# Kernel optimization log

Hardware: AMD Instinct MI355X
Metric: run time of the kernel (lower is better)

Reference implementation:

```python
import jax, jax.numpy as jnp
import numpy as np

H = 8          # num heads
LN_EPS = 1e-5  # torch LayerNorm default

_SHAPES = {
    'src': (1024, 8, 256), 'pos': (1024, 8, 256), 'query_embed': (80, 8, 256), 'cam_mask': (8, 80, 1024),
    'enc_qkv_w': (2, 768, 256), 'enc_qkv_b': (2, 768), 'enc_out_w': (2, 256, 256), 'enc_out_b': (2, 256),
    'enc_ln1_g': (2, 256), 'enc_ln1_b': (2, 256),
    'enc_ff1_w': (2, 2048, 256), 'enc_ff1_b': (2, 2048), 'enc_ff2_w': (2, 256, 2048), 'enc_ff2_b': (2, 256),
    'enc_ln2_g': (2, 256), 'enc_ln2_b': (2, 256),
    'dec_sa_qkv_w': (2, 768, 256), 'dec_sa_qkv_b': (2, 768), 'dec_sa_out_w': (2, 256, 256), 'dec_sa_out_b': (2, 256),
    'dec_ln1_g': (2, 256), 'dec_ln1_b': (2, 256),
    'dec_ca_qkv_w': (2, 768, 256), 'dec_ca_qkv_b': (2, 768), 'dec_ca_out_w': (2, 256, 256), 'dec_ca_out_b': (2, 256),
    'dec_ln2_g': (2, 256), 'dec_ln2_b': (2, 256),
    'dec_ff1_w': (2, 2048, 256), 'dec_ff1_b': (2, 2048), 'dec_ff2_w': (2, 256, 2048), 'dec_ff2_b': (2, 256),
    'dec_ln3_g': (2, 256), 'dec_ln3_b': (2, 256),
    'dec_norm_g': (256,), 'dec_norm_b': (256,),
}


def setup_inputs() -> dict:
    key = jax.random.key(0)
    out = {}
    for i, (name, sh) in enumerate(_SHAPES.items()):
        k = jax.random.fold_in(key, i)
        if name.endswith('_g'):
            out[name] = jnp.ones(sh, jnp.float32)
        elif name.endswith('ln1_b') or name.endswith('ln2_b') or name.endswith('ln3_b') or name == 'dec_norm_b':
            out[name] = jnp.zeros(sh, jnp.float32)
        else:
            scale = 1.0 if name in ('src', 'pos', 'query_embed', 'cam_mask') else 0.02
            out[name] = jax.random.normal(k, sh, dtype=jnp.float32) * scale
    return out


def layer_norm(x, g, b):
    mu = jnp.mean(x, axis=-1, keepdims=True)
    var = jnp.mean(jnp.square(x - mu), axis=-1, keepdims=True)
    return (x - mu) * jax.lax.rsqrt(var + LN_EPS) * g + b


def mha(q_in, k_in, v_in, qkv_w, qkv_b, out_w, out_b, bias=None):
    # q_in: [L,B,D], k_in/v_in: [S,B,D]; torch layout: projections are x @ W.T + b
    L, B, D = q_in.shape
    S = k_in.shape[0]
    hd = D // H
    wq, wk, wv = qkv_w[:D], qkv_w[D:2 * D], qkv_w[2 * D:]
    bq, bk, bv = qkv_b[:D], qkv_b[D:2 * D], qkv_b[2 * D:]
    q = (q_in @ wq.T + bq).reshape(L, B, H, hd).transpose(1, 2, 0, 3)  # [B,H,L,hd]
    k = (k_in @ wk.T + bk).reshape(S, B, H, hd).transpose(1, 2, 0, 3)  # [B,H,S,hd]
    v = (v_in @ wv.T + bv).reshape(S, B, H, hd).transpose(1, 2, 0, 3)
    logits = jnp.einsum('bhld,bhsd->bhls', q, k) * (1.0 / np.sqrt(hd))
    if bias is not None:
        logits = logits + bias[:, None, :, :]  # CAM bias broadcast over heads
    attn = jax.nn.softmax(logits, axis=-1)
    o = jnp.einsum('bhls,bhsd->bhld', attn, v).transpose(2, 0, 1, 3).reshape(L, B, D)
    return o @ out_w.T + out_b


def reference(src, pos, query_embed, cam_mask,
              enc_qkv_w, enc_qkv_b, enc_out_w, enc_out_b, enc_ln1_g, enc_ln1_b,
              enc_ff1_w, enc_ff1_b, enc_ff2_w, enc_ff2_b, enc_ln2_g, enc_ln2_b,
              dec_sa_qkv_w, dec_sa_qkv_b, dec_sa_out_w, dec_sa_out_b, dec_ln1_g, dec_ln1_b,
              dec_ca_qkv_w, dec_ca_qkv_b, dec_ca_out_w, dec_ca_out_b, dec_ln2_g, dec_ln2_b,
              dec_ff1_w, dec_ff1_b, dec_ff2_w, dec_ff2_b, dec_ln3_g, dec_ln3_b,
              dec_norm_g, dec_norm_b):
    n_enc = enc_qkv_w.shape[0]
    n_dec = dec_sa_qkv_w.shape[0]
    # --- encoder (post-norm DETR style, pos added to q,k) ---
    mem = src
    for i in range(n_enc):
        qk = mem + pos
        a = mha(qk, qk, mem, enc_qkv_w[i], enc_qkv_b[i], enc_out_w[i], enc_out_b[i])
        mem = layer_norm(mem + a, enc_ln1_g[i], enc_ln1_b[i])
        f = jax.nn.relu(mem @ enc_ff1_w[i].T + enc_ff1_b[i]) @ enc_ff2_w[i].T + enc_ff2_b[i]
        mem = layer_norm(mem + f, enc_ln2_g[i], enc_ln2_b[i])
    # --- decoder: tgt starts at zeros (Q2L), query_embed is query_pos ---
    tgt = jnp.zeros_like(query_embed)
    for i in range(n_dec):
        qk = tgt + query_embed
        sa = mha(qk, qk, tgt, dec_sa_qkv_w[i], dec_sa_qkv_b[i], dec_sa_out_w[i], dec_sa_out_b[i])
        tgt = layer_norm(tgt + sa, dec_ln1_g[i], dec_ln1_b[i])
        ca = mha(tgt + query_embed, mem + pos, mem,
                 dec_ca_qkv_w[i], dec_ca_qkv_b[i], dec_ca_out_w[i], dec_ca_out_b[i],
                 bias=cam_mask)  # MA: CAM-derived additive attention bias [B,L,S]
        tgt = layer_norm(tgt + ca, dec_ln2_g[i], dec_ln2_b[i])
        f = jax.nn.relu(tgt @ dec_ff1_w[i].T + dec_ff1_b[i]) @ dec_ff2_w[i].T + dec_ff2_b[i]
        tgt = layer_norm(tgt + f, dec_ln3_g[i], dec_ln3_b[i])
    out = layer_norm(tgt, dec_norm_g, dec_norm_b)
    return out[None]  # [1, L, B, D] as in TransformerDecoder's output.unsqueeze(0)
```

## Files before the change

### kernel.cpp

```cpp
#include <hip/hip_runtime.h>
#include <hip/hip_bf16.h>
#include <cstdint>
#include <cstddef>

typedef __hip_bfloat16 bf16;
typedef float f4 __attribute__((ext_vector_type(4)));
typedef float f32x4 __attribute__((ext_vector_type(4)));
typedef short s8v __attribute__((ext_vector_type(8)));
typedef unsigned short u16x4 __attribute__((ext_vector_type(4)));
typedef unsigned short u16x8 __attribute__((ext_vector_type(8)));

#define LN_EPS 1e-5f
#define LOG2E 1.4426950408889634f

#if __has_builtin(__builtin_amdgcn_exp2f)
__device__ __forceinline__ float EXP2(float x) { return __builtin_amdgcn_exp2f(x); }
#else
__device__ __forceinline__ float EXP2(float x) {
  float r; asm("v_exp_f32 %0, %1" : "=v"(r) : "v"(x)); return r;
}
#endif

__device__ __forceinline__ void async_cp16(const void* g, void* lds) {
  __builtin_amdgcn_global_load_lds(
      (const __attribute__((address_space(1))) unsigned int*)g,
      (__attribute__((address_space(3))) unsigned int*)lds, 16, 0, 0);
}

__device__ __forceinline__ uint32_t pkbf(float lo, float hi) {
#if __has_builtin(__builtin_amdgcn_perm)
  uint32_t l = __builtin_bit_cast(uint32_t, lo) + 0x8000u;
  uint32_t h = __builtin_bit_cast(uint32_t, hi) + 0x8000u;
  return __builtin_amdgcn_perm(h, l, 0x07060302u);
#else
  uint32_t l = __builtin_bit_cast(uint32_t, lo) + 0x8000u;
  uint32_t h = __builtin_bit_cast(uint32_t, hi) + 0x8000u;
  return (l >> 16) | (h & 0xFFFF0000u);
#endif
}

#define NCAST 16
struct CastArgs {
  const float* in[NCAST];
  bf16* out[NCAST];
  int end4[NCAST];
  int nseg;
};

__global__ __launch_bounds__(256) void cast_multi(CastArgs a, int total4) {
  int i = blockIdx.x * 256 + threadIdx.x;
  if (i >= total4) return;
  int s = 0;
  while (i >= a.end4[s]) ++s;
  int j = i - (s ? a.end4[s - 1] : 0);
  f4 v = ((const f4*)a.in[s])[j];
  u16x4 o;
#pragma unroll
  for (int c = 0; c < 4; ++c) {
    bf16 h = __float2bfloat16(v[c]);
    o[c] = *reinterpret_cast<unsigned short*>(&h);
  }
  ((u16x4*)a.out[s])[j] = o;
}

__global__ __launch_bounds__(256) void scale_f32_kernel(const float* __restrict__ in,
                                                        float* __restrict__ out,
                                                        float s, int n4) {
  int i = blockIdx.x * 256 + threadIdx.x;
  if (i < n4) {
    f4 v = ((const f4*)in)[i];
    ((f4*)out)[i] = v * s;
  }
}

__global__ __launch_bounds__(256) void add_bf16_kernel(const float* __restrict__ a,
                                                       const float* __restrict__ b,
                                                       bf16* __restrict__ out, int n4) {
  int i = blockIdx.x * 256 + threadIdx.x;
  if (i < n4) {
    f4 x = ((const f4*)a)[i];
    f4 y = ((const f4*)b)[i];
    u16x4 o;
#pragma unroll
    for (int j = 0; j < 4; ++j) {
      bf16 h = __float2bfloat16(x[j] + y[j]);
      o[j] = *reinterpret_cast<unsigned short*>(&h);
    }
    ((u16x4*)out)[i] = o;
  }
}

template <int TB, int MODE, int SPLITK>
__global__ __launch_bounds__(256, 2) void mfma_gemm(
    const bf16* __restrict__ A, const bf16* __restrict__ W,
    const float* __restrict__ bias, float* __restrict__ C,
    bf16* __restrict__ Cb, int M, int N, int K, int HL, float qscale) {
  constexpr int WM = TB / 2, WN = TB / 2;
  constexpr int MR = WM / 16, NR = WN / 16;
  constexpr int NCH = TB / 32;
  __shared__ __attribute__((aligned(16))) unsigned short SH[TB * 128];
  unsigned short (*As)[64] = (unsigned short(*)[64])SH;
  unsigned short (*Ws)[64] = (unsigned short(*)[64])(SH + TB * 64);
  const int tid = threadIdx.x;
  const int lane = tid & 63, wave = tid >> 6;
  const int wr = wave >> 1, wc = wave & 1;
  const int bm = blockIdx.x * TB, bn = blockIdx.y * TB;
  const int fr = lane & 15, fo = lane >> 4;
  const int srowi = lane >> 3;
  const int slot = lane & 7;
  const int gcol = (slot ^ srowi) * 8;

  const int kchunk = K / SPLITK;
  const int kbeg = (SPLITK > 1) ? blockIdx.z * kchunk : 0;

  f32x4 acc[MR][NR] = {};

  for (int k0 = kbeg; k0 < kbeg + kchunk; k0 += 64) {
    __syncthreads();
#pragma unroll
    for (int c = 0; c < NCH; ++c) {
      int rbase = wave * (TB / 4) + c * 8;
      int row = rbase + srowi;
      async_cp16(A + (size_t)(bm + row) * K + k0 + gcol, &As[rbase][0]);
      async_cp16(W + (size_t)(bn + row) * K + k0 + gcol, &Ws[rbase][0]);
    }
    __syncthreads();
#pragma unroll
    for (int ks = 0; ks < 2; ++ks) {
      s8v a[MR], b[NR];
#pragma unroll
      for (int mi = 0; mi < MR; ++mi) {
        int row = wr * WM + mi * 16 + fr;
        a[mi] = *(const s8v*)((const char*)&As[0][0] + row * 128 +
                              ((ks * 64 + fo * 16) ^ ((row & 7) << 4)));
      }
#pragma unroll
      for (int ni = 0; ni < NR; ++ni) {
        int row = wc * WN + ni * 16 + fr;
        b[ni] = *(const s8v*)((const char*)&Ws[0][0] + row * 128 +
                              ((ks * 64 + fo * 16) ^ ((row & 7) << 4)));
      }
#pragma unroll
      for (int mi = 0; mi < MR; ++mi)
#pragma unroll
        for (int ni = 0; ni < NR; ++ni)
          acc[mi][ni] = __builtin_amdgcn_mfma_f32_16x16x32_bf16(
              a[mi], b[ni], acc[mi][ni], 0, 0, 0);
    }
  }

  const int r0 = (lane >> 4) * 4;

  if (MODE == 5) {
    __syncthreads();
    unsigned short (*T)[72] = (unsigned short(*)[72])SH;
#pragma unroll
    for (int mi = 0; mi < MR; ++mi)
#pragma unroll
      for (int ni = 0; ni < NR; ++ni) {
        int colL = wc * WN + ni * 16 + fr;
        float bv = bias[bn + colL];
#pragma unroll
        for (int r = 0; r < 4; ++r) {
          int rowL = wr * WM + mi * 16 + r0 + r;
          bf16 hv = __float2bfloat16(acc[mi][ni][r] + bv);
          T[colL][rowL] = *(unsigned short*)&hv;
        }
      }
    __syncthreads();
    const int lbase = bm >> 3;
#pragma unroll
    for (int jj = 0; jj < 2; ++jj) {
      int cid = tid * 2 + jj;
      int colL = cid >> 3, bb = cid & 7;
      int c = bn + colL;
      int sec = c >> 8, hh = (c >> 5) & 7, d = c & 31;
      u16x8 v;
#pragma unroll
      for (int l = 0; l < 8; ++l) v[l] = T[colL][bb + 8 * l];
      *(u16x8*)(Cb + (size_t)sec * ((size_t)64 * 32 * HL) +
                ((size_t)(bb * 8 + hh) * 32 + d) * HL + lbase) = v;
    }
    return;
  }

  float* Cz = (MODE == 4) ? C + (size_t)blockIdx.z * M * N : C;
#pragma unroll
  for (int mi = 0; mi < MR; ++mi) {
#pragma unroll
    for (int ni = 0; ni < NR; ++ni) {
      int col = bn + wc * WN + ni * 16 + fr;
      float bv = (MODE == 4) ? 0.f : bias[col];
#pragma unroll
      for (int r = 0; r < 4; ++r) {
        int row = bm + wr * WM + mi * 16 + r0 + r;
        float t = acc[mi][ni][r] + bv;
        if (MODE == 2) t = fmaxf(t, 0.f);
        if (MODE == 0) {
          C[(size_t)row * N + col] = t;
        } else if (MODE == 4) {
          Cz[(size_t)row * N + col] = t;
        } else if (MODE == 3) {
          int l = row >> 3, bb = row & 7;
          int sec = col >> 8, hh = (col >> 5) & 7, d = col & 31;
          if (sec == 0) t *= qscale;
          Cb[(size_t)sec * ((size_t)64 * HL * 32) +
             ((size_t)(bb * 8 + hh) * HL + l) * 32 + d] = __float2bfloat16(t);
        } else {
          Cb[(size_t)row * N + col] = __float2bfloat16(t);
        }
      }
    }
  }
}

template <int HAS_BIAS, int PARTIAL, int NW>
__global__ __launch_bounds__(NW * 64, 4) void attn_mfma(
    const bf16* __restrict__ Qh, const bf16* __restrict__ Kh,
    const bf16* __restrict__ VhT, const float* __restrict__ bias,
    bf16* __restrict__ O, float* __restrict__ PO, float* __restrict__ PM,
    float* __restrict__ PL, int L, int S, int SC) {
  __shared__ __attribute__((aligned(16))) uint32_t Ps2[NW][16][36];
  const int tid = threadIdx.x;
  const int lane = tid & 63, wave = tid >> 6;
  const int fr = lane & 15, fo = lane >> 4;
  const int bh = blockIdx.x;
  const int b = bh >> 3, h = bh & 7;
  const int q0 = blockIdx.y * (NW * 16) + wave * 16;
  const int q = q0 + fr;

  const int cz = PARTIAL ? blockIdx.z : 0;
  const int sb = PARTIAL ? cz * SC : 0;
  const int se = PARTIAL ? min(S, sb + SC) : S;

  s8v qf = {};
  if (q < L) qf = *(const s8v*)(Qh + ((size_t)bh * L + q) * 32 + fo * 8);

  const float* brow = nullptr;
  if (HAS_BIAS) brow = bias + ((size_t)b * L + (q < L ? q : L - 1)) * S;

  float m = -1e30f, lsum = 0.f;
  f32x4 oacc[2] = {};

  s8v kf[4];
#pragma unroll
  for (int kb = 0; kb < 4; ++kb)
    kf[kb] = *(const s8v*)(Kh + ((size_t)bh * S + sb + kb * 16 + fr) * 32 + fo * 8);

  for (int s0 = sb; s0 < se; s0 += 64) {
    const bool more = (s0 + 64 < se);
    s8v kn[4];
    if (more) {
#pragma unroll
      for (int kb = 0; kb < 4; ++kb)
        kn[kb] = *(const s8v*)(Kh + ((size_t)bh * S + s0 + 64 + kb * 16 + fr) * 32 + fo * 8);
    }
    s8v vf[2][2];
#pragma unroll
    for (int dh = 0; dh < 2; ++dh)
#pragma unroll
      for (int ks = 0; ks < 2; ++ks)
        vf[dh][ks] = *(const s8v*)(VhT + ((size_t)bh * 32 + dh * 16 + fr) * S +
                                   s0 + ks * 32 + fo * 8);
    f4 bias4[4];
    if (HAS_BIAS) {
#pragma unroll
      for (int kb = 0; kb < 4; ++kb)
        bias4[kb] = *(const f4*)(brow + s0 + kb * 16 + 4 * fo);
    }

    f32x4 sa[4];
#pragma unroll
    for (int kb = 0; kb < 4; ++kb) {
      f32x4 z = {};
      sa[kb] = __builtin_amdgcn_mfma_f32_16x16x32_bf16(kf[kb], qf, z, 0, 0, 0);
    }

    float lg[16];
#pragma unroll
    for (int kb = 0; kb < 4; ++kb)
#pragma unroll
      for (int r = 0; r < 4; ++r)
        lg[kb * 4 + r] = HAS_BIAS ? sa[kb][r] + bias4[kb][r] : sa[kb][r];

    if (s0 + 64 > se) {
#pragma unroll
      for (int kb = 0; kb < 4; ++kb)
#pragma unroll
        for (int r = 0; r < 4; ++r)
          if (s0 + kb * 16 + 4 * fo + r >= se) lg[kb * 4 + r] = -1e30f;
    }

    float t0 = fmaxf(fmaxf(lg[0], lg[1]), fmaxf(lg[2], lg[3]));
    float t1 = fmaxf(fmaxf(lg[4], lg[5]), fmaxf(lg[6], lg[7]));
    float t2 = fmaxf(fmaxf(lg[8], lg[9]), fmaxf(lg[10], lg[11]));
    float t3 = fmaxf(fmaxf(lg[12], lg[13]), fmaxf(lg[14], lg[15]));
    float tm = fmaxf(fmaxf(t0, t1), fmaxf(t2, t3));
    tm = fmaxf(tm, __shfl_xor(tm, 16));
    tm = fmaxf(tm, __shfl_xor(tm, 32));

    if (__any(tm > m + 8.f)) {
      float nm = fmaxf(m, tm);
      float rs = EXP2(m - nm);
      m = nm;
      lsum *= rs;
#pragma unroll
      for (int r = 0; r < 4; ++r) { oacc[0][r] *= rs; oacc[1][r] *= rs; }
    }

    float pr[16];
    float ps = 0.f;
#pragma unroll
    for (int i = 0; i < 16; ++i) {
      pr[i] = EXP2(lg[i] - m);
      ps += pr[i];
    }
    lsum += ps;

#pragma unroll
    for (int kb = 0; kb < 4; ++kb) {
      uint32_t w0 = pkbf(pr[kb * 4 + 0], pr[kb * 4 + 1]);
      uint32_t w1 = pkbf(pr[kb * 4 + 2], pr[kb * 4 + 3]);
      uint64_t w = (uint64_t)w0 | ((uint64_t)w1 << 32);
      *(uint64_t*)&Ps2[wave][fr][kb * 8 + 2 * fo] = w;
    }

    s8v pf[2];
#pragma unroll
    for (int ks = 0; ks < 2; ++ks)
      pf[ks] = *(const s8v*)&Ps2[wave][fr][ks * 16 + 4 * fo];

#pragma unroll
    for (int dh = 0; dh < 2; ++dh)
#pragma unroll
      for (int ks = 0; ks < 2; ++ks)
        oacc[dh] = __builtin_amdgcn_mfma_f32_16x16x32_bf16(
            vf[dh][ks], pf[ks], oacc[dh], 0, 0, 0);

    if (more) {
#pragma unroll
      for (int kb = 0; kb < 4; ++kb) kf[kb] = kn[kb];
    }
  }

  lsum += __shfl_xor(lsum, 16);
  lsum += __shfl_xor(lsum, 32);

  if (q < L) {
    if (PARTIAL) {
      size_t pi = ((size_t)cz * 64 + bh) * L + q;
      float* po = PO + pi * 32;
#pragma unroll
      for (int dh = 0; dh < 2; ++dh) {
        f4 t;
#pragma unroll
        for (int r = 0; r < 4; ++r) t[r] = oacc[dh][r];
        *(f4*)(po + dh * 16 + 4 * fo) = t;
      }
      if (fo == 0) { PM[pi] = m; PL[pi] = lsum; }
    } else {
      float inv = 1.f / lsum;
      bf16* op = O + ((size_t)q * 8 + b) * 256 + h * 32;
#pragma unroll
      for (int dh = 0; dh < 2; ++dh) {
        uint32_t w0 = pkbf(oacc[dh][0] * inv, oacc[dh][1] * inv);
        uint32_t w1 = pkbf(oacc[dh][2] * inv, oacc[dh][3] * inv);
        *(uint32_t*)(op + dh * 16 + 4 * fo) = w0;
        *(uint32_t*)(op + dh * 16 + 4 * fo + 2) = w1;
      }
    }
  }
}

__global__ __launch_bounds__(256) void attn_combine(
    const float* __restrict__ PO, const float* __restrict__ PM,
    const float* __restrict__ PL, bf16* __restrict__ O, int L, int NC) {
  int gid = blockIdx.x * 256 + threadIdx.x;
  if (gid >= 64 * L * 32) return;
  int d = gid & 31;
  int rem = gid >> 5;
  int q = rem % L, bh = rem / L;
  int b = bh >> 3, h = bh & 7;
  float M = -1e30f;
  for (int c = 0; c < NC; ++c) M = fmaxf(M, PM[((size_t)c * 64 + bh) * L + q]);
  float lsum = 0.f, o = 0.f;
  for (int c = 0; c < NC; ++c) {
    size_t pi = ((size_t)c * 64 + bh) * L + q;
    float w = EXP2(PM[pi] - M);
    lsum += PL[pi] * w;
    o += PO[pi * 32 + d] * w;
  }
  O[((size_t)q * 8 + b) * 256 + h * 32 + d] = __float2bfloat16(o / lsum);
}

__global__ __launch_bounds__(256) void ln_kernel(
    const float* __restrict__ x, const float* __restrict__ res,
    const float* __restrict__ parts, int nparts, int pstride,
    const float* __restrict__ gbias,
    const float* __restrict__ g, const float* __restrict__ b,
    float* __restrict__ out, bf16* __restrict__ outb) {
  const int row = blockIdx.x, tid = threadIdx.x;
  size_t idx = (size_t)row * 256 + tid;
  float v = x[idx];
  if (res) v += res[idx];
  if (parts) {
    for (int z = 0; z < nparts; ++z) v += parts[(size_t)z * pstride + idx];
  }
  if (gbias) v += gbias[tid];
  float s = v, s2 = v * v;
#pragma unroll
  for (int off = 32; off >= 1; off >>= 1) {
    s += __shfl_down(s, off);
    s2 += __shfl_down(s2, off);
  }
  __shared__ float red[8];
  int wv = tid >> 6;
  if ((tid & 63) == 0) { red[wv] = s; red[4 + wv] = s2; }
  __syncthreads();
  if (tid == 0) {
    float ts = red[0] + red[1] + red[2] + red[3];
    float ts2 = red[4] + red[5] + red[6] + red[7];
    float mu = ts * (1.f / 256.f);
    float var = ts2 * (1.f / 256.f) - mu * mu;
    red[0] = mu;
    red[1] = rsqrtf(var + LN_EPS);
  }
  __syncthreads();
  float y = (v - red[0]) * red[1] * g[tid] + b[tid];
  if (out) out[idx] = y;
  if (outb) outb[idx] = __float2bfloat16(y);
}

extern "C" void kernel_launch(void* const* d_in, const int* in_sizes, int n_in,
                              void* d_out, int out_size, void* d_ws, size_t ws_size,
                              hipStream_t stream) {
  const float* src         = (const float*)d_in[0];
  const float* pos         = (const float*)d_in[1];
  const float* query_embed = (const float*)d_in[2];
  const float* cam_mask    = (const float*)d_in[3];
  const float* enc_qkv_w   = (const float*)d_in[4];
  const float* enc_qkv_b   = (const float*)d_in[5];
  const float* enc_out_w   = (const float*)d_in[6];
  const float* enc_out_b   = (const float*)d_in[7];
  const float* enc_ln1_g   = (const float*)d_in[8];
  const float* enc_ln1_b   = (const float*)d_in[9];
  const float* enc_ff1_w   = (const float*)d_in[10];
  const float* enc_ff1_b   = (const float*)d_in[11];
  const float* enc_ff2_w   = (const float*)d_in[12];
  const float* enc_ff2_b   = (const float*)d_in[13];
  const float* enc_ln2_g   = (const float*)d_in[14];
  const float* enc_ln2_b   = (const float*)d_in[15];
  const float* dec_sa_qkv_w= (const float*)d_in[16];
  const float* dec_sa_qkv_b= (const float*)d_in[17];
  const float* dec_sa_out_w= (const float*)d_in[18];
  const float* dec_sa_out_b= (const float*)d_in[19];
  const float* dec_ln1_g   = (const float*)d_in[20];
  const float* dec_ln1_b   = (const float*)d_in[21];
  const float* dec_ca_qkv_w= (const float*)d_in[22];
  const float* dec_ca_qkv_b= (const float*)d_in[23];
  const float* dec_ca_out_w= (const float*)d_in[24];
  const float* dec_ca_out_b= (const float*)d_in[25];
  const float* dec_ln2_g   = (const float*)d_in[26];
  const float* dec_ln2_b   = (const float*)d_in[27];
  const float* dec_ff1_w   = (const float*)d_in[28];
  const float* dec_ff1_b   = (const float*)d_in[29];
  const float* dec_ff2_w   = (const float*)d_in[30];
  const float* dec_ff2_b   = (const float*)d_in[31];
  const float* dec_ln3_g   = (const float*)d_in[32];
  const float* dec_ln3_b   = (const float*)d_in[33];
  const float* dec_norm_g  = (const float*)d_in[34];
  const float* dec_norm_b  = (const float*)d_in[35];

  size_t off = 0;
  char* base = (char*)d_ws;
  auto af = [&](size_t n) { float* p = (float*)(base + off); off += n * 4; return p; };
  auto ab = [&](size_t n) { bf16*  p = (bf16*)(base + off);  off += n * 2; return p; };

  float* mem  = af(2097152);
  float* r1   = af(2097152);
  float* PO   = af(8388608);
  float* pm   = af(262144);
  float* pl   = af(262144);
  float* cmlog= af(655360);
  float* pb   = af(1024);
  float* tgt  = af(163840);
  float* tpr  = af(163840);
  bf16* memb  = ab(2097152);
  bf16* qkb   = ab(2097152);
  bf16* aob   = ab(2097152);
  bf16* ffb   = ab(16777216);
  bf16* bufQ  = ab(4194304);
  bf16* bufK  = ab(4194304);
  bf16* bufV  = ab(4194304);
  bf16* bufVsa= ab(163840);
  bf16* tgtb  = ab(163840);
  bf16* tqkb  = ab(163840);
  bf16* taob  = ab(163840);
  bf16* tffb  = ab(1310720);
  bf16* w_enc_qkv = ab(393216);
  bf16* w_enc_out = ab(131072);
  bf16* w_enc_ff1 = ab(1048576);
  bf16* w_enc_ff2 = ab(1048576);
  bf16* w_sa_qkv  = ab(393216);
  bf16* w_sa_out  = ab(131072);
  bf16* w_ca_q    = ab(131072);
  bf16* w_ca_kv   = ab(262144);
  bf16* w_ca_out  = ab(131072);
  bf16* w_dec_ff1 = ab(1048576);
  bf16* w_dec_ff2 = ab(1048576);

  const float qscale = 0.17677669529663687f * LOG2E;

  {
    CastArgs ca;
    const float* ins[NCAST] = {
        enc_qkv_w, enc_out_w, enc_ff1_w, enc_ff2_w,
        dec_sa_qkv_w, dec_sa_out_w,
        dec_ca_qkv_w,
        dec_ca_qkv_w + 65536,
        dec_ca_qkv_w + 131072,
        dec_ca_qkv_w + 196608,
        dec_ca_qkv_w + 262144,
        dec_ca_qkv_w + 327680,
        dec_ca_out_w, dec_ff1_w, dec_ff2_w, src};
    bf16* outs[NCAST] = {
        w_enc_qkv, w_enc_out, w_enc_ff1, w_enc_ff2,
        w_sa_qkv, w_sa_out,
        w_ca_q,
        w_ca_kv,
        w_ca_kv + 131072,
        w_ca_q + 65536,
        w_ca_kv + 65536,
        w_ca_kv + 196608,
        w_ca_out, w_dec_ff1, w_dec_ff2, memb};
    int n4s[NCAST] = {98304, 32768, 262144, 262144, 98304, 32768,
                      16384, 16384, 16384, 16384, 16384, 16384,
                      32768, 262144, 262144, 524288};
    int acc = 0;
    for (int s = 0; s < NCAST; ++s) {
      ca.in[s] = ins[s]; ca.out[s] = outs[s];
      acc += n4s[s]; ca.end4[s] = acc;
    }
    ca.nseg = NCAST;
    cast_multi<<<(acc + 255) / 256, 256, 0, stream>>>(ca, acc);
  }
  scale_f32_kernel<<<640, 256, 0, stream>>>(cam_mask, cmlog, LOG2E, 163840);
  hipMemcpyAsync(mem, src, (size_t)2097152 * 4, hipMemcpyDeviceToDevice, stream);
  hipMemcpyAsync(pb,       dec_ca_qkv_b + 256,       1024, hipMemcpyDeviceToDevice, stream);
  hipMemcpyAsync(pb + 256, dec_ca_qkv_b + 768 + 256, 1024, hipMemcpyDeviceToDevice, stream);
  hipMemcpyAsync(pb + 512, dec_ca_qkv_b + 512,       1024, hipMemcpyDeviceToDevice, stream);
  hipMemcpyAsync(pb + 768, dec_ca_qkv_b + 768 + 512, 1024, hipMemcpyDeviceToDevice, stream);

  auto g64_f = [&](const bf16* A, const bf16* W, const float* bias, float* C,
                   int M, int N, int K) {
    mfma_gemm<64, 0, 1><<<dim3(M / 64, N / 64), 256, 0, stream>>>(
        A, W, bias, C, nullptr, M, N, K, 0, 1.f);
  };
  auto g64_head = [&](const bf16* A, const bf16* W, const float* bias, bf16* Cb,
                      int M, int N, int K, int HL, float qs) {
    mfma_gemm<64, 3, 1><<<dim3(M / 64, N / 64), 256, 0, stream>>>(
        A, W, bias, nullptr, Cb, M, N, K, HL, qs);
  };
  auto g64_headT = [&](const bf16* A, const bf16* W, const float* bias, bf16* Cb,
                       int M, int N, int K, int HL) {
    mfma_gemm<64, 5, 1><<<dim3(M / 64, N / 64), 256, 0, stream>>>(
        A, W, bias, nullptr, Cb, M, N, K, HL, 1.f);
  };
  auto g64_relu = [&](const bf16* A, const bf16* W, const float* bias, bf16* Cb,
                      int M, int N, int K) {
    mfma_gemm<64, 2, 1><<<dim3(M / 64, N / 64), 256, 0, stream>>>(
        A, W, bias, nullptr, Cb, M, N, K, 0, 1.f);
  };
  auto g128_relu = [&](const bf16* A, const bf16* W, const float* bias, bf16* Cb,
                       int M, int N, int K) {
    mfma_gemm<128, 2, 1><<<dim3(M / 128, N / 128), 256, 0, stream>>>(
        A, W, bias, nullptr, Cb, M, N, K, 0, 1.f);
  };

  for (int i = 0; i < 2; ++i) {
    const bf16* wq = w_enc_qkv + (size_t)i * 196608;
    const float* qkvb = enc_qkv_b + (size_t)i * 768;
    add_bf16_kernel<<<2048, 256, 0, stream>>>(mem, pos, qkb, 524288);
    g64_head(qkb, wq, qkvb, bufQ, 8192, 512, 256, 1024, qscale);
    g64_headT(memb, wq + 131072, qkvb + 512, bufV, 8192, 256, 256, 1024);
    attn_mfma<0, 0, 4><<<dim3(64, 16), 256, 0, stream>>>(
        bufQ, bufQ + 2097152, bufV, nullptr, aob, nullptr, nullptr, nullptr,
        1024, 1024, 0);
    g64_f(aob, w_enc_out + (size_t)i * 65536, enc_out_b + i * 256, r1,
          8192, 256, 256);
    ln_kernel<<<8192, 256, 0, stream>>>(mem, r1, nullptr, 0, 0, nullptr,
                                        enc_ln1_g + i * 256, enc_ln1_b + i * 256,
                                        mem, memb);
    g128_relu(memb, w_enc_ff1 + (size_t)i * 524288, enc_ff1_b + i * 2048, ffb,
              8192, 2048, 256);
    mfma_gemm<128, 4, 4><<<dim3(64, 2, 4), 256, 0, stream>>>(
        ffb, w_enc_ff2 + (size_t)i * 524288, nullptr, PO, nullptr,
        8192, 256, 2048, 0, 1.f);
    ln_kernel<<<8192, 256, 0, stream>>>(mem, nullptr, PO, 4, 2097152,
                                        enc_ff2_b + i * 256,
                                        enc_ln2_g + i * 256, enc_ln2_b + i * 256,
                                        mem, memb);
  }

  hipMemsetAsync(tgt, 0, (size_t)163840 * 4, stream);
  hipMemsetAsync(tgtb, 0, (size_t)163840 * 2, stream);
  add_bf16_kernel<<<2048, 256, 0, stream>>>(mem, pos, qkb, 524288);

  g64_head(qkb, w_ca_kv, pb, bufK, 8192, 512, 256, 1024, 1.f);
  g64_headT(memb, w_ca_kv + 131072, pb + 512, bufV, 8192, 512, 256, 1024);

  for (int i = 0; i < 2; ++i) {
    const bf16* wsa = w_sa_qkv + (size_t)i * 196608;
    const float* sab = dec_sa_qkv_b + (size_t)i * 768;
    const float* cab = dec_ca_qkv_b + (size_t)i * 768;

    add_bf16_kernel<<<160, 256, 0, stream>>>(tgt, query_embed, tqkb, 40960);
    g64_head(tqkb, wsa, sab, bufQ, 640, 512, 256, 80, qscale);
    g64_headT(tgtb, wsa + 131072, sab + 512, bufVsa, 640, 256, 256, 80);
    attn_mfma<0, 0, 1><<<dim3(64, 5), 64, 0, stream>>>(
        bufQ, bufQ + 163840, bufVsa, nullptr, taob, nullptr, nullptr, nullptr,
        80, 80, 0);
    g64_f(taob, w_sa_out + (size_t)i * 65536, dec_sa_out_b + i * 256, tpr,
          640, 256, 256);
    ln_kernel<<<640, 256, 0, stream>>>(tgt, tpr, nullptr, 0, 0, nullptr,
                                       dec_ln1_g + i * 256, dec_ln1_b + i * 256,
                                       tgt, tgtb);
    add_bf16_kernel<<<160, 256, 0, stream>>>(tgt, query_embed, tqkb, 40960);
    g64_head(tqkb, w_ca_q + (size_t)i * 65536, cab, bufQ, 640, 256, 256, 80, qscale);
    attn_mfma<1, 1, 1><<<dim3(64, 5, 8), 64, 0, stream>>>(
        bufQ, bufK + (size_t)i * 2097152, bufV + (size_t)i * 2097152, cmlog,
        nullptr, PO, pm, pl, 80, 1024, 128);
    attn_combine<<<640, 256, 0, stream>>>(PO, pm, pl, taob, 80, 8);
    g64_f(taob, w_ca_out + (size_t)i * 65536, dec_ca_out_b + i * 256, tpr,
          640, 256, 256);
    ln_kernel<<<640, 256, 0, stream>>>(tgt, tpr, nullptr, 0, 0, nullptr,
                                       dec_ln2_g + i * 256, dec_ln2_b + i * 256,
                                       tgt, tgtb);
    g64_relu(tgtb, w_dec_ff1 + (size_t)i * 524288, dec_ff1_b + i * 2048, tffb,
             640, 2048, 256);
    mfma_gemm<64, 4, 4><<<dim3(10, 4, 4), 256, 0, stream>>>(
        tffb, w_dec_ff2 + (size_t)i * 524288, nullptr, PO, nullptr,
        640, 256, 2048, 0, 1.f);
    ln_kernel<<<640, 256, 0, stream>>>(tgt, nullptr, PO, 4, 163840,
                                       dec_ff2_b + i * 256,
                                       dec_ln3_g + i * 256, dec_ln3_b + i * 256,
                                       tgt, tgtb);
  }

  ln_kernel<<<640, 256, 0, stream>>>(tgt, nullptr, nullptr, 0, 0, nullptr,
                                     dec_norm_g, dec_norm_b,
                                     (float*)d_out, nullptr);
}
```

Baseline: 431.8 us.

## Software-pipeline attention loop: overlap next tile's QK softmax with current PV

Restructures the attention inner loop so the QK^T MFMA and softmax for the next 64-key tile run after the PV MFMA of the current tile. P is double-buffered in LDS and the rescale factor is carried forward. The lazy rescale (skip unless the max grew by more than 8) is replaced with an unconditional one. V tiles are also prefetched one step ahead. This aims to hide MFMA and exp latency behind each other, at the cost of more registers and extra LDS. The bufVsa allocation grows slightly, probably because the prefetch can read past the end of the buffer.

```diff
diff --git a/kernel.cpp b/kernel.cpp
--- a/kernel.cpp
+++ b/kernel.cpp
@@ -220,7 +220,7 @@
     const bf16* __restrict__ VhT, const float* __restrict__ bias,
     bf16* __restrict__ O, float* __restrict__ PO, float* __restrict__ PM,
     float* __restrict__ PL, int L, int S, int SC) {
-  __shared__ __attribute__((aligned(16))) uint32_t Ps2[NW][16][36];
+  __shared__ __attribute__((aligned(16))) uint32_t Ps2[NW][2][16][36];
   const int tid = threadIdx.x;
   const int lane = tid & 63, wave = tid >> 6;
   const int fr = lane & 15, fo = lane >> 4;
@@ -232,6 +232,7 @@
   const int cz = PARTIAL ? blockIdx.z : 0;
   const int sb = PARTIAL ? cz * SC : 0;
   const int se = PARTIAL ? min(S, sb + SC) : S;
+  const int ng = (se - sb + 63) >> 6;
 
   s8v qf = {};
   if (q < L) qf = *(const s8v*)(Qh + ((size_t)bh * L + q) * 32 + fo * 8);
@@ -239,58 +240,57 @@
   const float* brow = nullptr;
   if (HAS_BIAS) brow = bias + ((size_t)b * L + (q < L ? q : L - 1)) * S;
 
+  const bf16* Kbase = Kh + (size_t)bh * S * 32;
+  const bf16* Vbase = VhT + (size_t)bh * 32 * S;
+
   float m = -1e30f, lsum = 0.f;
   f32x4 oacc[2] = {};
 
-  s8v kf[4];
-#pragma unroll
-  for (int kb = 0; kb < 4; ++kb)
-    kf[kb] = *(const s8v*)(Kh + ((size_t)bh * S + sb + kb * 16 + fr) * 32 + fo * 8);
-
-  for (int s0 = sb; s0 < se; s0 += 64) {
-    const bool more = (s0 + 64 < se);
-    s8v kn[4];
-    if (more) {
-#pragma unroll
-      for (int kb = 0; kb < 4; ++kb)
-        kn[kb] = *(const s8v*)(Kh + ((size_t)bh * S + s0 + 64 + kb * 16 + fr) * 32 + fo * 8);
-    }
-    s8v vf[2][2];
+  s8v kn[4], vf[2][2], vn[2][2];
+  float lg[16];
+  f4 bias4[4];
+
+  auto loadK = [&](s8v* dst, int s0) {
+#pragma unroll
+    for (int kb = 0; kb < 4; ++kb)
+      dst[kb] = *(const s8v*)(Kbase + (size_t)(s0 + kb * 16 + fr) * 32 + fo * 8);
+  };
+  auto loadV = [&](s8v (*dst)[2], int s0) {
 #pragma unroll
     for (int dh = 0; dh < 2; ++dh)
 #pragma unroll
       for (int ks = 0; ks < 2; ++ks)
-        vf[dh][ks] = *(const s8v*)(VhT + ((size_t)bh * 32 + dh * 16 + fr) * S +
-                                   s0 + ks * 32 + fo * 8);
-    f4 bias4[4];
+        dst[dh][ks] = *(const s8v*)(Vbase + (size_t)(dh * 16 + fr) * S +
+                                    s0 + ks * 32 + fo * 8);
+  };
+  auto loadB = [&](int s0) {
     if (HAS_BIAS) {
 #pragma unroll
       for (int kb = 0; kb < 4; ++kb)
         bias4[kb] = *(const f4*)(brow + s0 + kb * 16 + 4 * fo);
     }
-
-    f32x4 sa[4];
+  };
+  auto qk = [&](const s8v* kfr) {
 #pragma unroll
     for (int kb = 0; kb < 4; ++kb) {
       f32x4 z = {};
-      sa[kb] = __builtin_amdgcn_mfma_f32_16x16x32_bf16(kf[kb], qf, z, 0, 0, 0);
-    }
-
-    float lg[16];
-#pragma unroll
-    for (int kb = 0; kb < 4; ++kb)
-#pragma unroll
-      for (int r = 0; r < 4; ++r)
-        lg[kb * 4 + r] = HAS_BIAS ? sa[kb][r] + bias4[kb][r] : sa[kb][r];
-
+      f32x4 sa = __builtin_amdgcn_mfma_f32_16x16x32_bf16(kfr[kb], qf, z, 0, 0, 0);
+#pragma unroll
+      for (int r = 0; r < 4; ++r) lg[kb * 4 + r] = sa[r];
+    }
+  };
+  auto softmax_pack = [&](int s0, int bufi) -> float {
+    if (HAS_BIAS) {
+#pragma unroll
+      for (int i = 0; i < 16; ++i) lg[i] += bias4[i >> 2][i & 3];
+    }
     if (s0 + 64 > se) {
 #pragma unroll
-      for (int kb = 0; kb < 4; ++kb)
-#pragma unroll
-        for (int r = 0; r < 4; ++r)
-          if (s0 + kb * 16 + 4 * fo + r >= se) lg[kb * 4 + r] = -1e30f;
-    }
-
+      for (int i = 0; i < 16; ++i) {
+        int key = s0 + (i >> 2) * 16 + 4 * fo + (i & 3);
+        if (key >= se) lg[i] = -1e30f;
+      }
+    }
     float t0 = fmaxf(fmaxf(lg[0], lg[1]), fmaxf(lg[2], lg[3]));
     float t1 = fmaxf(fmaxf(lg[4], lg[5]), fmaxf(lg[6], lg[7]));
     float t2 = fmaxf(fmaxf(lg[8], lg[9]), fmaxf(lg[10], lg[11]));
@@ -298,48 +298,59 @@
     float tm = fmaxf(fmaxf(t0, t1), fmaxf(t2, t3));
     tm = fmaxf(tm, __shfl_xor(tm, 16));
     tm = fmaxf(tm, __shfl_xor(tm, 32));
-
-    if (__any(tm > m + 8.f)) {
-      float nm = fmaxf(m, tm);
-      float rs = EXP2(m - nm);
-      m = nm;
-      lsum *= rs;
-#pragma unroll
-      for (int r = 0; r < 4; ++r) { oacc[0][r] *= rs; oacc[1][r] *= rs; }
-    }
-
-    float pr[16];
+    float nm = fmaxf(m, tm);
+    float rs = EXP2(m - nm);
+    m = nm;
     float ps = 0.f;
 #pragma unroll
     for (int i = 0; i < 16; ++i) {
-      pr[i] = EXP2(lg[i] - m);
-      ps += pr[i];
-    }
-    lsum += ps;
-
+      lg[i] = EXP2(lg[i] - nm);
+      ps += lg[i];
+    }
+    lsum = lsum * rs + ps;
 #pragma unroll
     for (int kb = 0; kb < 4; ++kb) {
-      uint32_t w0 = pkbf(pr[kb * 4 + 0], pr[kb * 4 + 1]);
-      uint32_t w1 = pkbf(pr[kb * 4 + 2], pr[kb * 4 + 3]);
+      uint32_t w0 = pkbf(lg[kb * 4 + 0], lg[kb * 4 + 1]);
+      uint32_t w1 = pkbf(lg[kb * 4 + 2], lg[kb * 4 + 3]);
       uint64_t w = (uint64_t)w0 | ((uint64_t)w1 << 32);
-      *(uint64_t*)&Ps2[wave][fr][kb * 8 + 2 * fo] = w;
-    }
-
+      *(uint64_t*)&Ps2[wave][bufi][fr][kb * 8 + 2 * fo] = w;
+    }
+    return rs;
+  };
+
+  loadK(kn, sb);
+  loadV(vf, sb);
+  loadB(sb);
+  qk(kn);
+  float pend_rs = softmax_pack(sb, 0);
+
+  for (int g = 0; g < ng; ++g) {
+    const bool more = (g + 1 < ng);
+    const int s_next = sb + (g + 1) * 64;
+    if (more) {
+      loadK(kn, s_next);
+      loadV(vn, s_next);
+      loadB(s_next);
+    }
+#pragma unroll
+    for (int r = 0; r < 4; ++r) { oacc[0][r] *= pend_rs; oacc[1][r] *= pend_rs; }
     s8v pf[2];
 #pragma unroll
     for (int ks = 0; ks < 2; ++ks)
-      pf[ks] = *(const s8v*)&Ps2[wave][fr][ks * 16 + 4 * fo];
-
+      pf[ks] = *(const s8v*)&Ps2[wave][g & 1][fr][ks * 16 + 4 * fo];
 #pragma unroll
     for (int dh = 0; dh < 2; ++dh)
 #pragma unroll
       for (int ks = 0; ks < 2; ++ks)
         oacc[dh] = __builtin_amdgcn_mfma_f32_16x16x32_bf16(
             vf[dh][ks], pf[ks], oacc[dh], 0, 0, 0);
-
     if (more) {
-#pragma unroll
-      for (int kb = 0; kb < 4; ++kb) kf[kb] = kn[kb];
+      qk(kn);
+      pend_rs = softmax_pack(s_next, (g + 1) & 1);
+#pragma unroll
+      for (int dh = 0; dh < 2; ++dh)
+#pragma unroll
+        for (int ks = 0; ks < 2; ++ks) vf[dh][ks] = vn[dh][ks];
     }
   }
 
@@ -352,10 +363,10 @@
       float* po = PO + pi * 32;
 #pragma unroll
       for (int dh = 0; dh < 2; ++dh) {
-        f4 t;
-#pragma unroll
-        for (int r = 0; r < 4; ++r) t[r] = oacc[dh][r];
-        *(f4*)(po + dh * 16 + 4 * fo) = t;
+        f4 t2;
+#pragma unroll
+        for (int r = 0; r < 4; ++r) t2[r] = oacc[dh][r];
+        *(f4*)(po + dh * 16 + 4 * fo) = t2;
       }
       if (fo == 0) { PM[pi] = m; PL[pi] = lsum; }
     } else {
@@ -492,7 +503,7 @@
   bf16* bufQ  = ab(4194304);
   bf16* bufK  = ab(4194304);
   bf16* bufV  = ab(4194304);
-  bf16* bufVsa= ab(163840);
+  bf16* bufVsa= ab(172032);
   bf16* tgtb  = ab(163840);
   bf16* tqkb  = ab(163840);
   bf16* taob  = ab(163840);
```

New measurement: 433.4 us. About the same (+0.4%).
